# Optimization experiments

Measured on AMD Instinct MI355X. Metric: run time of the kernel, lower is better.

## Reference

```python
import jax, jax.numpy as jnp
import numpy as np

# Plane axes from generate_planes(); projection uses their inverses (permutation matrices).
_PLANES = np.array([[[1, 0, 0], [0, 1, 0], [0, 0, 1]],
                    [[1, 0, 0], [0, 0, 1], [0, 1, 0]],
                    [[0, 0, 1], [1, 0, 0], [0, 1, 0]]], dtype=np.float32)
_INV_PLANES = np.linalg.inv(_PLANES)  # [3,3,3]


def _grid_sample_2d(feat, grid):
    """Bilinear grid_sample, padding_mode='zeros', align_corners=False.
    feat: [C,H,W], grid: [M,2] with (x,y) in normalized coords. Returns [C,M]."""
    C, H, W = feat.shape
    x = ((grid[:, 0] + 1.0) * W - 1.0) * 0.5  # [M] pixel coords
    y = ((grid[:, 1] + 1.0) * H - 1.0) * 0.5
    x0 = jnp.floor(x)
    y0 = jnp.floor(y)
    wx = x - x0  # weight of right/bottom neighbor
    wy = y - y0
    x0i = x0.astype(jnp.int32)
    y0i = y0.astype(jnp.int32)
    x1i = x0i + 1
    y1i = y0i + 1

    def corner(xi, yi):
        valid = (xi >= 0) & (xi < W) & (yi >= 0) & (yi < H)
        xc = jnp.clip(xi, 0, W - 1)
        yc = jnp.clip(yi, 0, H - 1)
        v = feat[:, yc, xc]  # [C, M] gather
        return v * valid.astype(feat.dtype)

    v00 = corner(x0i, y0i)
    v10 = corner(x1i, y0i)
    v01 = corner(x0i, y1i)
    v11 = corner(x1i, y1i)
    out = (v00 * (1.0 - wx) * (1.0 - wy)
           + v10 * wx * (1.0 - wy)
           + v01 * (1.0 - wx) * wy
           + v11 * wx * wy)
    return out  # [C, M]


def setup_inputs() -> dict:
    key = jax.random.key(0)
    k1, k2, k3 = jax.random.split(key, 3)
    N, P, C, H, W, M = 4, 3, 32, 256, 256, 500000
    planes = jax.random.normal(k1, (N, P, C, H, W), dtype=jnp.float32)
    sample_coordinates = jax.random.uniform(k2, (N, M, 3), dtype=jnp.float32,
                                            minval=-1.0, maxval=1.0)
    sample_directions = jax.random.normal(k3, (N, M, 3), dtype=jnp.float32)
    return {"planes": planes, "sample_coordinates": sample_coordinates,
            "sample_directions": sample_directions}


def reference(planes, sample_coordinates, sample_directions):
    # ImportanceRenderer.run_model: project -> grid_sample per plane -> mean over planes.
    N, n_planes, C, H, W = planes.shape
    M = sample_coordinates.shape[1]
    inv = jnp.asarray(_INV_PLANES, dtype=sample_coordinates.dtype)  # [P,3,3]
    # torch.bmm(coords, inv_planes): [N,P,M,3] @ [P,3,3] -> take first 2 dims
    proj = jnp.einsum('nmi,pij->npmj', sample_coordinates, inv)[..., :2]  # [N,P,M,2]
    feats = planes.reshape(N * n_planes, C, H, W)
    grids = proj.reshape(N * n_planes, M, 2)
    sampled = jax.vmap(_grid_sample_2d)(feats, grids)  # [N*P, C, M]
    sampled = sampled.reshape(N, n_planes, C, M).transpose(0, 1, 3, 2)  # [N,P,M,C]
    return sampled.mean(axis=1)  # [N, M, C]
```

## Files before the change

kernel.cpp:

```cpp
#include <hip/hip_runtime.h>
#include <hip/hip_fp16.h>


constexpr int Cc = 32, Hh = 256, Ww = 256, Pp = 3, Nn = 4;
constexpr int HWPIX = Hh * Ww;

__global__ __launch_bounds__(256) void transpose_chw_hwc_h(
    const float* __restrict__ in, __half* __restrict__ out)
{
    __shared__ float lds[Cc * 257];
    const int slice = blockIdx.y;
    const int pix0  = blockIdx.x * 256;
    const int t     = threadIdx.x;

    const float* src = in + (size_t)slice * Cc * HWPIX + pix0 + t;
    #pragma unroll
    for (int c = 0; c < Cc; ++c)
        lds[c * 257 + t] = src[(size_t)c * HWPIX];
    __syncthreads();

    uint4* dst = reinterpret_cast<uint4*>(
        out + (size_t)slice * HWPIX * Cc + (size_t)pix0 * Cc);
    #pragma unroll
    for (int k = 0; k < 4; ++k) {
        const int idx = k * 256 + t;
        const int pix = idx >> 2;
        const int c0  = (idx & 3) * 8;
        unsigned r[4];
        #pragma unroll
        for (int j = 0; j < 4; ++j) {
            const __half h0 = __float2half(lds[(c0 + 2 * j + 0) * 257 + pix]);
            const __half h1 = __float2half(lds[(c0 + 2 * j + 1) * 257 + pix]);
            r[j] = (unsigned)__half_as_ushort(h0)
                 | ((unsigned)__half_as_ushort(h1) << 16);
        }
        dst[idx] = make_uint4(r[0], r[1], r[2], r[3]);
    }
}

__global__ __launch_bounds__(256) void triplane_gather_hwc8h(
    const __half* __restrict__ tp, const float* __restrict__ coords,
    float* __restrict__ out, int M)
{
    const int gid   = blockIdx.x * 256 + threadIdx.x;
    const int m     = gid >> 3;
    const int chunk = gid & 7;
    const int n     = blockIdx.y;
    if (m >= M) return;

    const float* cp = coords + ((size_t)n * M + m) * 3;
    const float cx = cp[0], cy = cp[1], cz = cp[2];

    const uint2* addr[12];
    float w[12];

    #pragma unroll
    for (int p = 0; p < 3; ++p) {
        const float gx = (p == 2) ? cz : cx;
        const float gy = (p == 0) ? cy : ((p == 1) ? cz : cx);
        const float x = ((gx + 1.0f) * 256.0f - 1.0f) * 0.5f;
        const float y = ((gy + 1.0f) * 256.0f - 1.0f) * 0.5f;
        const float x0f = floorf(x), y0f = floorf(y);
        const float wx = x - x0f, wy = y - y0f;
        const int x0 = (int)x0f, y0 = (int)y0f;
        const int x1 = x0 + 1,   y1 = y0 + 1;
        const bool vx0 = (unsigned)x0 < 256u;
        const bool vx1 = (unsigned)x1 < 256u;
        const bool vy0 = (unsigned)y0 < 256u;
        const bool vy1 = (unsigned)y1 < 256u;
        const int cx0 = min(max(x0, 0), 255), cx1 = min(max(x1, 0), 255);
        const int cy0 = min(max(y0, 0), 255), cy1 = min(max(y1, 0), 255);

        w[p * 4 + 0] = ((vx0 && vy0) ? 1.f : 0.f) * (1.f - wx) * (1.f - wy);
        w[p * 4 + 1] = ((vx1 && vy0) ? 1.f : 0.f) * wx * (1.f - wy);
        w[p * 4 + 2] = ((vx0 && vy1) ? 1.f : 0.f) * (1.f - wx) * wy;
        w[p * 4 + 3] = ((vx1 && vy1) ? 1.f : 0.f) * wx * wy;

        const uint2* base = reinterpret_cast<const uint2*>(
            tp + (size_t)(n * 3 + p) * HWPIX * Cc);
        addr[p * 4 + 0] = base + (size_t)((cy0 << 8) + cx0) * 8 + chunk;
        addr[p * 4 + 1] = base + (size_t)((cy0 << 8) + cx1) * 8 + chunk;
        addr[p * 4 + 2] = base + (size_t)((cy1 << 8) + cx0) * 8 + chunk;
        addr[p * 4 + 3] = base + (size_t)((cy1 << 8) + cx1) * 8 + chunk;
    }

    uint2 rv[12];
    #pragma unroll
    for (int j = 0; j < 12; ++j) rv[j] = *addr[j];

    float4 acc = make_float4(0.f, 0.f, 0.f, 0.f);
    #pragma unroll
    for (int j = 0; j < 12; ++j) {
        const __half2 h0 = *reinterpret_cast<const __half2*>(&rv[j].x);
        const __half2 h1 = *reinterpret_cast<const __half2*>(&rv[j].y);
        const float2 f0 = __half22float2(h0);
        const float2 f1 = __half22float2(h1);
        acc.x += w[j] * f0.x;
        acc.y += w[j] * f0.y;
        acc.z += w[j] * f1.x;
        acc.w += w[j] * f1.y;
    }

    constexpr float third = 1.0f / 3.0f;
    acc.x *= third; acc.y *= third; acc.z *= third; acc.w *= third;

    float4* op = reinterpret_cast<float4*>(out + ((size_t)n * M + m) * Cc);
    op[chunk] = acc;
}

__global__ __launch_bounds__(256) void triplane_gather_chw(
    const float* __restrict__ planes, const float* __restrict__ coords,
    float* __restrict__ out, int M)
{
    const int m = blockIdx.x * 256 + threadIdx.x;
    const int n = blockIdx.y;
    if (m >= M) return;

    const float* cp = coords + ((size_t)n * M + m) * 3;
    const float cx = cp[0], cy = cp[1], cz = cp[2];

    int   off[3][4];
    float w[3][4];
    #pragma unroll
    for (int p = 0; p < 3; ++p) {
        const float gx = (p == 2) ? cz : cx;
        const float gy = (p == 0) ? cy : ((p == 1) ? cz : cx);
        const float x = ((gx + 1.0f) * 256.0f - 1.0f) * 0.5f;
        const float y = ((gy + 1.0f) * 256.0f - 1.0f) * 0.5f;
        const float x0f = floorf(x), y0f = floorf(y);
        const float wx = x - x0f, wy = y - y0f;
        const int x0 = (int)x0f, y0 = (int)y0f;
        const int x1 = x0 + 1,   y1 = y0 + 1;
        const bool vx0 = (unsigned)x0 < 256u, vx1 = (unsigned)x1 < 256u;
        const bool vy0 = (unsigned)y0 < 256u, vy1 = (unsigned)y1 < 256u;
        const int cx0 = min(max(x0, 0), 255), cx1 = min(max(x1, 0), 255);
        const int cy0 = min(max(y0, 0), 255), cy1 = min(max(y1, 0), 255);
        off[p][0] = (cy0 << 8) + cx0;  w[p][0] = ((vx0 && vy0) ? 1.f : 0.f) * (1.f - wx) * (1.f - wy);
        off[p][1] = (cy0 << 8) + cx1;  w[p][1] = ((vx1 && vy0) ? 1.f : 0.f) * wx * (1.f - wy);
        off[p][2] = (cy1 << 8) + cx0;  w[p][2] = ((vx0 && vy1) ? 1.f : 0.f) * (1.f - wx) * wy;
        off[p][3] = (cy1 << 8) + cx1;  w[p][3] = ((vx1 && vy1) ? 1.f : 0.f) * wx * wy;
    }

    float* op = out + ((size_t)n * M + m) * Cc;
    constexpr float third = 1.0f / 3.0f;
    for (int c = 0; c < Cc; ++c) {
        float a = 0.f;
        #pragma unroll
        for (int p = 0; p < 3; ++p) {
            const float* b = planes + ((size_t)(n * 3 + p) * Cc + c) * HWPIX;
            a += w[p][0] * b[off[p][0]] + w[p][1] * b[off[p][1]]
               + w[p][2] * b[off[p][2]] + w[p][3] * b[off[p][3]];
        }
        op[c] = a * third;
    }
}

extern "C" void kernel_launch(void* const* d_in, const int* in_sizes, int n_in,
                              void* d_out, int out_size, void* d_ws, size_t ws_size,
                              hipStream_t stream)
{
    const float* planes = (const float*)d_in[0];
    const float* coords = (const float*)d_in[1];
    float* out = (float*)d_out;

    const int M = in_sizes[1] / (Nn * 3);
    const size_t need = (size_t)Nn * Pp * HWPIX * Cc * sizeof(__half);

    if (ws_size >= need) {
        __half* tp = (__half*)d_ws;
        transpose_chw_hwc_h<<<dim3(HWPIX / 256, Nn * Pp), 256, 0, stream>>>(planes, tp);
        const int gx = (M * 8 + 255) / 256;
        triplane_gather_hwc8h<<<dim3(gx, Nn), 256, 0, stream>>>(tp, coords, out, M);
    } else {
        const int gx = (M + 255) / 256;
        triplane_gather_chw<<<dim3(gx, Nn), 256, 0, stream>>>(planes, coords, out, M);
    }
}
```

Before: 291.0 us.

## Sort sample points by Morton cell before triplane gather for cache locality

Adds a counting sort of sample points into 32^3 Morton-ordered cells (histogram, scan, atomic scatter) and a new gather kernel that reads the sorted records and writes results back to their original indices. Spatially close points then hit nearby texels in all three planes, which is meant to raise L2/MALL hit rates on the random gathers. It also remaps block IDs so that contiguous work lands on the same XCD. The cost is four extra kernel launches, atomics, an extra workspace buffer, and scattered output writes. The new path runs only if the workspace is large enough, otherwise it falls back to the old kernels.

```diff
diff --git a/kernel.cpp b/kernel.cpp
--- a/kernel.cpp
+++ b/kernel.cpp
@@ -4,6 +4,22 @@
 
 constexpr int Cc = 32, Hh = 256, Ww = 256, Pp = 3, Nn = 4;
 constexpr int HWPIX = Hh * Ww;
+constexpr int NCELLS = 32768;
+
+__device__ inline unsigned spread3(unsigned x) {
+    x &= 0x3FFu;
+    x = (x | (x << 16)) & 0x030000FFu;
+    x = (x | (x << 8))  & 0x0300F00Fu;
+    x = (x | (x << 4))  & 0x030C30C3u;
+    x = (x | (x << 2))  & 0x09249249u;
+    return x;
+}
+__device__ inline unsigned morton_key(float cx, float cy, float cz) {
+    const int a = min(max((int)((cx + 1.0f) * 16.0f), 0), 31);
+    const int b = min(max((int)((cy + 1.0f) * 16.0f), 0), 31);
+    const int c = min(max((int)((cz + 1.0f) * 16.0f), 0), 31);
+    return spread3((unsigned)a) | (spread3((unsigned)b) << 1) | (spread3((unsigned)c) << 2);
+}
 
 __global__ __launch_bounds__(256) void transpose_chw_hwc_h(
     const float* __restrict__ in, __half* __restrict__ out)
@@ -38,28 +54,91 @@
     }
 }
 
-__global__ __launch_bounds__(256) void triplane_gather_hwc8h(
-    const __half* __restrict__ tp, const float* __restrict__ coords,
-    float* __restrict__ out, int M)
-{
-    const int gid   = blockIdx.x * 256 + threadIdx.x;
-    const int m     = gid >> 3;
-    const int chunk = gid & 7;
-    const int n     = blockIdx.y;
+__global__ __launch_bounds__(256) void zero_u32(unsigned* __restrict__ p, int n)
+{
+    const int i = blockIdx.x * 256 + threadIdx.x;
+    if (i < n) p[i] = 0u;
+}
+
+__global__ __launch_bounds__(256) void hist_kernel(
+    const float* __restrict__ coords, unsigned* __restrict__ hist, int M)
+{
+    const int m = blockIdx.x * 256 + threadIdx.x;
+    const int n = blockIdx.y;
     if (m >= M) return;
-
+    const float* cp = coords + ((size_t)n * M + m) * 3;
+    const unsigned key = morton_key(cp[0], cp[1], cp[2]);
+    atomicAdd(&hist[n * NCELLS + key], 1u);
+}
+
+__global__ __launch_bounds__(1024) void scan_kernel(unsigned* __restrict__ hist)
+{
+    __shared__ unsigned lds[1024];
+    unsigned* h = hist + (size_t)blockIdx.x * NCELLS;
+    const int t = threadIdx.x;
+    unsigned v[32];
+    unsigned s = 0;
+    #pragma unroll
+    for (int i = 0; i < 32; ++i) { v[i] = h[t * 32 + i]; s += v[i]; }
+    lds[t] = s;
+    __syncthreads();
+    for (int d = 1; d < 1024; d <<= 1) {
+        const unsigned add = (t >= d) ? lds[t - d] : 0u;
+        __syncthreads();
+        lds[t] += add;
+        __syncthreads();
+    }
+    unsigned base = (t > 0) ? lds[t - 1] : 0u;
+    #pragma unroll
+    for (int i = 0; i < 32; ++i) { const unsigned tmp = v[i]; h[t * 32 + i] = base; base += tmp; }
+}
+
+__global__ __launch_bounds__(256) void scatter_kernel(
+    const float* __restrict__ coords, unsigned* __restrict__ hist,
+    float4* __restrict__ rec, int M)
+{
+    const int m = blockIdx.x * 256 + threadIdx.x;
+    const int n = blockIdx.y;
+    if (m >= M) return;
     const float* cp = coords + ((size_t)n * M + m) * 3;
     const float cx = cp[0], cy = cp[1], cz = cp[2];
+    const unsigned key = morton_key(cx, cy, cz);
+    const unsigned pos = atomicAdd(&hist[n * NCELLS + key], 1u);
+    float4 r;
+    r.x = cx; r.y = cy; r.z = cz; r.w = __int_as_float(m);
+    rec[(size_t)n * M + pos] = r;
+}
+
+__global__ __launch_bounds__(256) void triplane_gather_sorted(
+    const __half* __restrict__ tp, const float4* __restrict__ rec,
+    float* __restrict__ out, int M, int gx, int nwg)
+{
+    int bid = blockIdx.x;
+    {
+        const int q = nwg >> 3, r = nwg & 7;
+        const int xcd = bid & 7, idx = bid >> 3;
+        bid = (xcd < r ? xcd * (q + 1) : r * (q + 1) + (xcd - r) * q) + idx;
+    }
+    const int n  = bid / gx;
+    const int bx = bid - n * gx;
+    const int gid   = bx * 256 + threadIdx.x;
+    const int s     = gid >> 3;
+    const int chunk = gid & 7;
+    if (s >= M) return;
+
+    const float4 rc = rec[(size_t)n * M + s];
+    const float cx = rc.x, cy = rc.y, cz = rc.z;
+    const int   m  = __float_as_int(rc.w);
 
     const uint2* addr[12];
     float w[12];
 
     #pragma unroll
     for (int p = 0; p < 3; ++p) {
-        const float gx = (p == 2) ? cz : cx;
-        const float gy = (p == 0) ? cy : ((p == 1) ? cz : cx);
-        const float x = ((gx + 1.0f) * 256.0f - 1.0f) * 0.5f;
-        const float y = ((gy + 1.0f) * 256.0f - 1.0f) * 0.5f;
+        const float gxc = (p == 2) ? cz : cx;
+        const float gyc = (p == 0) ? cy : ((p == 1) ? cz : cx);
+        const float x = ((gxc + 1.0f) * 256.0f - 1.0f) * 0.5f;
+        const float y = ((gyc + 1.0f) * 256.0f - 1.0f) * 0.5f;
         const float x0f = floorf(x), y0f = floorf(y);
         const float wx = x - x0f, wy = y - y0f;
         const int x0 = (int)x0f, y0 = (int)y0f;
@@ -108,6 +187,76 @@
     op[chunk] = acc;
 }
 
+__global__ __launch_bounds__(256) void triplane_gather_hwc8h(
+    const __half* __restrict__ tp, const float* __restrict__ coords,
+    float* __restrict__ out, int M)
+{
+    const int gid   = blockIdx.x * 256 + threadIdx.x;
+    const int m     = gid >> 3;
+    const int chunk = gid & 7;
+    const int n     = blockIdx.y;
+    if (m >= M) return;
+
+    const float* cp = coords + ((size_t)n * M + m) * 3;
+    const float cx = cp[0], cy = cp[1], cz = cp[2];
+
+    const uint2* addr[12];
+    float w[12];
+
+    #pragma unroll
+    for (int p = 0; p < 3; ++p) {
+        const float gxc = (p == 2) ? cz : cx;
+        const float gyc = (p == 0) ? cy : ((p == 1) ? cz : cx);
+        const float x = ((gxc + 1.0f) * 256.0f - 1.0f) * 0.5f;
+        const float y = ((gyc + 1.0f) * 256.0f - 1.0f) * 0.5f;
+        const float x0f = floorf(x), y0f = floorf(y);
+        const float wx = x - x0f, wy = y - y0f;
+        const int x0 = (int)x0f, y0 = (int)y0f;
+        const int x1 = x0 + 1,   y1 = y0 + 1;
+        const bool vx0 = (unsigned)x0 < 256u;
+        const bool vx1 = (unsigned)x1 < 256u;
+        const bool vy0 = (unsigned)y0 < 256u;
+        const bool vy1 = (unsigned)y1 < 256u;
+        const int cx0 = min(max(x0, 0), 255), cx1 = min(max(x1, 0), 255);
+        const int cy0 = min(max(y0, 0), 255), cy1 = min(max(y1, 0), 255);
+
+        w[p * 4 + 0] = ((vx0 && vy0) ? 1.f : 0.f) * (1.f - wx) * (1.f - wy);
+        w[p * 4 + 1] = ((vx1 && vy0) ? 1.f : 0.f) * wx * (1.f - wy);
+        w[p * 4 + 2] = ((vx0 && vy1) ? 1.f : 0.f) * (1.f - wx) * wy;
+        w[p * 4 + 3] = ((vx1 && vy1) ? 1.f : 0.f) * wx * wy;
+
+        const uint2* base = reinterpret_cast<const uint2*>(
+            tp + (size_t)(n * 3 + p) * HWPIX * Cc);
+        addr[p * 4 + 0] = base + (size_t)((cy0 << 8) + cx0) * 8 + chunk;
+        addr[p * 4 + 1] = base + (size_t)((cy0 << 8) + cx1) * 8 + chunk;
+        addr[p * 4 + 2] = base + (size_t)((cy1 << 8) + cx0) * 8 + chunk;
+        addr[p * 4 + 3] = base + (size_t)((cy1 << 8) + cx1) * 8 + chunk;
+    }
+
+    uint2 rv[12];
+    #pragma unroll
+    for (int j = 0; j < 12; ++j) rv[j] = *addr[j];
+
+    float4 acc = make_float4(0.f, 0.f, 0.f, 0.f);
+    #pragma unroll
+    for (int j = 0; j < 12; ++j) {
+        const __half2 h0 = *reinterpret_cast<const __half2*>(&rv[j].x);
+        const __half2 h1 = *reinterpret_cast<const __half2*>(&rv[j].y);
+        const float2 f0 = __half22float2(h0);
+        const float2 f1 = __half22float2(h1);
+        acc.x += w[j] * f0.x;
+        acc.y += w[j] * f0.y;
+        acc.z += w[j] * f1.x;
+        acc.w += w[j] * f1.y;
+    }
+
+    constexpr float third = 1.0f / 3.0f;
+    acc.x *= third; acc.y *= third; acc.z *= third; acc.w *= third;
+
+    float4* op = reinterpret_cast<float4*>(out + ((size_t)n * M + m) * Cc);
+    op[chunk] = acc;
+}
+
 __global__ __launch_bounds__(256) void triplane_gather_chw(
     const float* __restrict__ planes, const float* __restrict__ coords,
     float* __restrict__ out, int M)
@@ -123,10 +272,10 @@
     float w[3][4];
     #pragma unroll
     for (int p = 0; p < 3; ++p) {
-        const float gx = (p == 2) ? cz : cx;
-        const float gy = (p == 0) ? cy : ((p == 1) ? cz : cx);
-        const float x = ((gx + 1.0f) * 256.0f - 1.0f) * 0.5f;
-        const float y = ((gy + 1.0f) * 256.0f - 1.0f) * 0.5f;
+        const float gxc = (p == 2) ? cz : cx;
+        const float gyc = (p == 0) ? cy : ((p == 1) ? cz : cx);
+        const float x = ((gxc + 1.0f) * 256.0f - 1.0f) * 0.5f;
+        const float y = ((gyc + 1.0f) * 256.0f - 1.0f) * 0.5f;
         const float x0f = floorf(x), y0f = floorf(y);
         const float wx = x - x0f, wy = y - y0f;
         const int x0 = (int)x0f, y0 = (int)y0f;
@@ -164,9 +313,26 @@
     float* out = (float*)d_out;
 
     const int M = in_sizes[1] / (Nn * 3);
-    const size_t need = (size_t)Nn * Pp * HWPIX * Cc * sizeof(__half);
-
-    if (ws_size >= need) {
+
+    const size_t tp_bytes   = (size_t)Nn * Pp * HWPIX * Cc * sizeof(__half);
+    const size_t rec_bytes  = (size_t)Nn * M * sizeof(float4);
+    const size_t hist_bytes = (size_t)Nn * NCELLS * sizeof(unsigned);
+
+    if (ws_size >= tp_bytes + rec_bytes + hist_bytes) {
+        __half*   tp   = (__half*)d_ws;
+        float4*   rec  = (float4*)((char*)d_ws + tp_bytes);
+        unsigned* hist = (unsigned*)((char*)d_ws + tp_bytes + rec_bytes);
+
+        transpose_chw_hwc_h<<<dim3(HWPIX / 256, Nn * Pp), 256, 0, stream>>>(planes, tp);
+        zero_u32<<<(Nn * NCELLS + 255) / 256, 256, 0, stream>>>(hist, Nn * NCELLS);
+        hist_kernel<<<dim3((M + 255) / 256, Nn), 256, 0, stream>>>(coords, hist, M);
+        scan_kernel<<<Nn, 1024, 0, stream>>>(hist);
+        scatter_kernel<<<dim3((M + 255) / 256, Nn), 256, 0, stream>>>(coords, hist, rec, M);
+
+        const int gx  = (M * 8 + 255) / 256;
+        const int nwg = Nn * gx;
+        triplane_gather_sorted<<<nwg, 256, 0, stream>>>(tp, rec, out, M, gx, nwg);
+    } else if (ws_size >= tp_bytes) {
         __half* tp = (__half*)d_ws;
         transpose_chw_hwc_h<<<dim3(HWPIX / 256, Nn * Pp), 256, 0, stream>>>(planes, tp);
         const int gx = (M * 8 + 255) / 256;
```

Measured after the change: 403.2 us. +38.6%, slower.

## Bin samples by Morton-ordered coarse cells before gathering for cache locality

Applied to the files above, without the earlier changes.

Adds a pre-pass that buckets each sample into one of 4096 coarse 3D cells (Morton key), with per-cell capacity and an overflow tail. The gather kernel then processes samples in bin order, so nearby texels are reused in cache. It also remaps block IDs across the XCDs, uses 4 threads per sample with two loads each, and accumulates in half-precision FMA. Costs are extra kernels, atomics, a sparse slot grid with many idle threads (NCO*CAP slots plus M), scattered output writes, and reduced precision from fp16 weights and accumulation.

```diff
diff --git a/kernel.cpp b/kernel.cpp
--- a/kernel.cpp
+++ b/kernel.cpp
@@ -4,6 +4,23 @@
 
 constexpr int Cc = 32, Hh = 256, Ww = 256, Pp = 3, Nn = 4;
 constexpr int HWPIX = Hh * Ww;
+constexpr int NCO   = 4096;
+constexpr int CAP   = 160;
+
+__device__ inline unsigned spread3(unsigned x) {
+    x &= 0x3FFu;
+    x = (x | (x << 16)) & 0x030000FFu;
+    x = (x | (x << 8))  & 0x0300F00Fu;
+    x = (x | (x << 4))  & 0x030C30C3u;
+    x = (x | (x << 2))  & 0x09249249u;
+    return x;
+}
+__device__ inline unsigned coarse_key(float cx, float cy, float cz) {
+    const int a = min(max((int)((cx + 1.0f) * 8.0f), 0), 15);
+    const int b = min(max((int)((cy + 1.0f) * 8.0f), 0), 15);
+    const int c = min(max((int)((cz + 1.0f) * 8.0f), 0), 15);
+    return spread3((unsigned)a) | (spread3((unsigned)b) << 1) | (spread3((unsigned)c) << 2);
+}
 
 __global__ __launch_bounds__(256) void transpose_chw_hwc_h(
     const float* __restrict__ in, __half* __restrict__ out)
@@ -38,28 +55,75 @@
     }
 }
 
-__global__ __launch_bounds__(256) void triplane_gather_hwc8h(
-    const __half* __restrict__ tp, const float* __restrict__ coords,
-    float* __restrict__ out, int M)
-{
-    const int gid   = blockIdx.x * 256 + threadIdx.x;
-    const int m     = gid >> 3;
-    const int chunk = gid & 7;
-    const int n     = blockIdx.y;
+__global__ __launch_bounds__(256) void zero_u32(unsigned* __restrict__ p, int n)
+{
+    const int i = blockIdx.x * 256 + threadIdx.x;
+    if (i < n) p[i] = 0u;
+}
+
+__global__ __launch_bounds__(256) void bin_scatter(
+    const float* __restrict__ coords, unsigned* __restrict__ count,
+    unsigned* __restrict__ tailcnt, unsigned* __restrict__ idx,
+    unsigned* __restrict__ tail, int M)
+{
+    const int m = blockIdx.x * 256 + threadIdx.x;
+    const int n = blockIdx.y;
     if (m >= M) return;
+    const float* cp = coords + ((size_t)n * M + m) * 3;
+    const unsigned k = coarse_key(cp[0], cp[1], cp[2]);
+    const unsigned r = atomicAdd(&count[n * NCO + k], 1u);
+    if (r < CAP) {
+        idx[((size_t)n * NCO + k) * CAP + r] = (unsigned)m;
+    } else {
+        const unsigned t = atomicAdd(&tailcnt[n], 1u);
+        tail[(size_t)n * M + t] = (unsigned)m;
+    }
+}
+
+__global__ __launch_bounds__(256) void triplane_gather_binned(
+    const __half* __restrict__ tp, const unsigned* __restrict__ count,
+    const unsigned* __restrict__ tailcnt, const unsigned* __restrict__ idx,
+    const unsigned* __restrict__ tail, const float* __restrict__ coords,
+    float* __restrict__ out, int M, int slots, int gx, int nwg)
+{
+    int bid = blockIdx.x;
+    {
+        const int q = nwg >> 3, r = nwg & 7;
+        const int xcd = bid & 7, i = bid >> 3;
+        bid = (xcd < r ? xcd * (q + 1) : r * (q + 1) + (xcd - r) * q) + i;
+    }
+    const int n  = bid / gx;
+    const int bx = bid - n * gx;
+    const int gid  = bx * 256 + threadIdx.x;
+    const int s    = gid >> 2;
+    const int quad = gid & 3;
+    if (s >= slots) return;
+
+    int m;
+    if (s < NCO * CAP) {
+        const int cell = s / CAP;
+        const int r    = s - cell * CAP;
+        const unsigned cnt = count[n * NCO + cell];
+        if ((unsigned)r >= cnt) return;
+        m = (int)idx[(size_t)n * NCO * CAP + s];
+    } else {
+        const int t = s - NCO * CAP;
+        if ((unsigned)t >= tailcnt[n]) return;
+        m = (int)tail[(size_t)n * M + t];
+    }
 
     const float* cp = coords + ((size_t)n * M + m) * 3;
     const float cx = cp[0], cy = cp[1], cz = cp[2];
 
     const uint2* addr[12];
-    float w[12];
+    __half2 wh[12];
 
     #pragma unroll
     for (int p = 0; p < 3; ++p) {
-        const float gx = (p == 2) ? cz : cx;
-        const float gy = (p == 0) ? cy : ((p == 1) ? cz : cx);
-        const float x = ((gx + 1.0f) * 256.0f - 1.0f) * 0.5f;
-        const float y = ((gy + 1.0f) * 256.0f - 1.0f) * 0.5f;
+        const float gxc = (p == 2) ? cz : cx;
+        const float gyc = (p == 0) ? cy : ((p == 1) ? cz : cx);
+        const float x = ((gxc + 1.0f) * 256.0f - 1.0f) * 0.5f;
+        const float y = ((gyc + 1.0f) * 256.0f - 1.0f) * 0.5f;
         const float x0f = floorf(x), y0f = floorf(y);
         const float wx = x - x0f, wy = y - y0f;
         const int x0 = (int)x0f, y0 = (int)y0f;
@@ -71,6 +135,98 @@
         const int cx0 = min(max(x0, 0), 255), cx1 = min(max(x1, 0), 255);
         const int cy0 = min(max(y0, 0), 255), cy1 = min(max(y1, 0), 255);
 
+        const float w00 = ((vx0 && vy0) ? 1.f : 0.f) * (1.f - wx) * (1.f - wy);
+        const float w10 = ((vx1 && vy0) ? 1.f : 0.f) * wx * (1.f - wy);
+        const float w01 = ((vx0 && vy1) ? 1.f : 0.f) * (1.f - wx) * wy;
+        const float w11 = ((vx1 && vy1) ? 1.f : 0.f) * wx * wy;
+        wh[p * 4 + 0] = __float2half2_rn(w00);
+        wh[p * 4 + 1] = __float2half2_rn(w10);
+        wh[p * 4 + 2] = __float2half2_rn(w01);
+        wh[p * 4 + 3] = __float2half2_rn(w11);
+
+        const uint2* base = reinterpret_cast<const uint2*>(
+            tp + (size_t)(n * 3 + p) * HWPIX * Cc);
+        addr[p * 4 + 0] = base + (size_t)((cy0 << 8) + cx0) * 8 + quad;
+        addr[p * 4 + 1] = base + (size_t)((cy0 << 8) + cx1) * 8 + quad;
+        addr[p * 4 + 2] = base + (size_t)((cy1 << 8) + cx0) * 8 + quad;
+        addr[p * 4 + 3] = base + (size_t)((cy1 << 8) + cx1) * 8 + quad;
+    }
+
+    uint2 lo[12], hi[12];
+    #pragma unroll
+    for (int j = 0; j < 12; ++j) lo[j] = addr[j][0];
+    #pragma unroll
+    for (int j = 0; j < 12; ++j) hi[j] = addr[j][4];
+
+    float accA[4], accB[4];
+    #pragma unroll
+    for (int i = 0; i < 4; ++i) { accA[i] = 0.f; accB[i] = 0.f; }
+
+    #pragma unroll
+    for (int p = 0; p < 3; ++p) {
+        __half2 a0 = __float2half2_rn(0.f), a1 = a0, b0 = a0, b1 = a0;
+        #pragma unroll
+        for (int c = 0; c < 4; ++c) {
+            const int j = p * 4 + c;
+            const __half2 w = wh[j];
+            a0 = __hfma2(*reinterpret_cast<const __half2*>(&lo[j].x), w, a0);
+            a1 = __hfma2(*reinterpret_cast<const __half2*>(&lo[j].y), w, a1);
+            b0 = __hfma2(*reinterpret_cast<const __half2*>(&hi[j].x), w, b0);
+            b1 = __hfma2(*reinterpret_cast<const __half2*>(&hi[j].y), w, b1);
+        }
+        const float2 f0 = __half22float2(a0);
+        const float2 f1 = __half22float2(a1);
+        const float2 g0 = __half22float2(b0);
+        const float2 g1 = __half22float2(b1);
+        accA[0] += f0.x; accA[1] += f0.y; accA[2] += f1.x; accA[3] += f1.y;
+        accB[0] += g0.x; accB[1] += g0.y; accB[2] += g1.x; accB[3] += g1.y;
+    }
+
+    constexpr float third = 1.0f / 3.0f;
+    float4 oA, oB;
+    oA.x = accA[0] * third; oA.y = accA[1] * third;
+    oA.z = accA[2] * third; oA.w = accA[3] * third;
+    oB.x = accB[0] * third; oB.y = accB[1] * third;
+    oB.z = accB[2] * third; oB.w = accB[3] * third;
+
+    float4* op = reinterpret_cast<float4*>(out + ((size_t)n * M + m) * Cc);
+    op[quad]     = oA;
+    op[quad + 4] = oB;
+}
+
+__global__ __launch_bounds__(256) void triplane_gather_hwc8h(
+    const __half* __restrict__ tp, const float* __restrict__ coords,
+    float* __restrict__ out, int M)
+{
+    const int gid   = blockIdx.x * 256 + threadIdx.x;
+    const int m     = gid >> 3;
+    const int chunk = gid & 7;
+    const int n     = blockIdx.y;
+    if (m >= M) return;
+
+    const float* cp = coords + ((size_t)n * M + m) * 3;
+    const float cx = cp[0], cy = cp[1], cz = cp[2];
+
+    const uint2* addr[12];
+    float w[12];
+
+    #pragma unroll
+    for (int p = 0; p < 3; ++p) {
+        const float gxc = (p == 2) ? cz : cx;
+        const float gyc = (p == 0) ? cy : ((p == 1) ? cz : cx);
+        const float x = ((gxc + 1.0f) * 256.0f - 1.0f) * 0.5f;
+        const float y = ((gyc + 1.0f) * 256.0f - 1.0f) * 0.5f;
+        const float x0f = floorf(x), y0f = floorf(y);
+        const float wx = x - x0f, wy = y - y0f;
+        const int x0 = (int)x0f, y0 = (int)y0f;
+        const int x1 = x0 + 1,   y1 = y0 + 1;
+        const bool vx0 = (unsigned)x0 < 256u;
+        const bool vx1 = (unsigned)x1 < 256u;
+        const bool vy0 = (unsigned)y0 < 256u;
+        const bool vy1 = (unsigned)y1 < 256u;
+        const int cx0 = min(max(x0, 0), 255), cx1 = min(max(x1, 0), 255);
+        const int cy0 = min(max(y0, 0), 255), cy1 = min(max(y1, 0), 255);
+
         w[p * 4 + 0] = ((vx0 && vy0) ? 1.f : 0.f) * (1.f - wx) * (1.f - wy);
         w[p * 4 + 1] = ((vx1 && vy0) ? 1.f : 0.f) * wx * (1.f - wy);
         w[p * 4 + 2] = ((vx0 && vy1) ? 1.f : 0.f) * (1.f - wx) * wy;
@@ -123,10 +279,10 @@
     float w[3][4];
     #pragma unroll
     for (int p = 0; p < 3; ++p) {
-        const float gx = (p == 2) ? cz : cx;
-        const float gy = (p == 0) ? cy : ((p == 1) ? cz : cx);
-        const float x = ((gx + 1.0f) * 256.0f - 1.0f) * 0.5f;
-        const float y = ((gy + 1.0f) * 256.0f - 1.0f) * 0.5f;
+        const float gxc = (p == 2) ? cz : cx;
+        const float gyc = (p == 0) ? cy : ((p == 1) ? cz : cx);
+        const float x = ((gxc + 1.0f) * 256.0f - 1.0f) * 0.5f;
+        const float y = ((gyc + 1.0f) * 256.0f - 1.0f) * 0.5f;
         const float x0f = floorf(x), y0f = floorf(y);
         const float wx = x - x0f, wy = y - y0f;
         const int x0 = (int)x0f, y0 = (int)y0f;
@@ -164,9 +320,34 @@
     float* out = (float*)d_out;
 
     const int M = in_sizes[1] / (Nn * 3);
-    const size_t need = (size_t)Nn * Pp * HWPIX * Cc * sizeof(__half);
-
-    if (ws_size >= need) {
+
+    auto align256 = [](size_t x) { return (x + 255) & ~(size_t)255; };
+    const size_t tph_bytes  = align256((size_t)Nn * Pp * HWPIX * Cc * sizeof(__half));
+    const size_t idx_bytes  = align256((size_t)Nn * NCO * CAP * sizeof(unsigned));
+    const size_t tail_bytes = align256((size_t)Nn * M * sizeof(unsigned));
+    const size_t cnt_bytes  = align256((size_t)Nn * NCO * sizeof(unsigned));
+    const size_t tc_bytes   = align256((size_t)Nn * sizeof(unsigned));
+
+    if (ws_size >= tph_bytes + idx_bytes + tail_bytes + cnt_bytes + tc_bytes) {
+        char* p = (char*)d_ws;
+        __half*   tp      = (__half*)p;   p += tph_bytes;
+        unsigned* idx     = (unsigned*)p; p += idx_bytes;
+        unsigned* tail    = (unsigned*)p; p += tail_bytes;
+        unsigned* count   = (unsigned*)p; p += cnt_bytes;
+        unsigned* tailcnt = (unsigned*)p;
+
+        transpose_chw_hwc_h<<<dim3(HWPIX / 256, Nn * Pp), 256, 0, stream>>>(planes, tp);
+        zero_u32<<<(Nn * NCO + 255) / 256, 256, 0, stream>>>(count, Nn * NCO);
+        zero_u32<<<1, 256, 0, stream>>>(tailcnt, Nn);
+        bin_scatter<<<dim3((M + 255) / 256, Nn), 256, 0, stream>>>(
+            coords, count, tailcnt, idx, tail, M);
+
+        const int slots = NCO * CAP + M;
+        const int gx    = (slots * 4 + 255) / 256;
+        const int nwg   = Nn * gx;
+        triplane_gather_binned<<<nwg, 256, 0, stream>>>(
+            tp, count, tailcnt, idx, tail, coords, out, M, slots, gx, nwg);
+    } else if (ws_size >= tph_bytes) {
         __half* tp = (__half*)d_ws;
         transpose_chw_hwc_h<<<dim3(HWPIX / 256, Nn * Pp), 256, 0, stream>>>(planes, tp);
         const int gx = (M * 8 + 255) / 256;
```

New measurement: 404.6 us. 39.1% more time.
